# Optimization experiments

Measured on AMD Instinct MI355X. Metric: run time of the kernel, lower is better.

The kernel has to match this reference:

```python
import jax, jax.numpy as jnp
import numpy as np

C, V, T, B = 64, 16000, 64, 8
ALPHA = 1.0  # dt=None -> alpha = 1 (non-trainable buffer)


def setup_inputs() -> dict:
    key = jax.random.key(0)
    k0, k1, k2, k3 = jax.random.split(key, 4)
    tokens = jax.random.randint(k0, (T, B), 0, V)  # time-major [T, B]
    emb_ctx = jax.random.normal(k1, (V, C), dtype=jnp.float32)  # embedding2context
    emb_act = jax.random.normal(k2, (V, C), dtype=jnp.float32)  # embedding2actionable
    bound = 1.0 / np.sqrt(C)
    W_a = jax.random.uniform(k3, (C * V, C), dtype=jnp.float32, minval=-bound, maxval=bound)
    beta_mult = jnp.float32(1.0)
    beta_power = jnp.float32(1.0)
    return {"tokens": tokens, "emb_ctx": emb_ctx, "emb_act": emb_act,
            "W_a": W_a, "beta_mult": beta_mult, "beta_power": beta_power}


def reference(tokens, emb_ctx, emb_act, W_a, beta_mult, beta_power):
    Vv, Cc = emb_ctx.shape
    Tt, Bb = tokens.shape
    # W_a rows are indexed k = v*C + c after .view(-1, V, C)
    W3 = W_a.reshape(Vv, Cc, Cc)  # [V, C, C]

    def step(ctx, tok):
        ce = emb_ctx[tok]  # [B, C] context embedding
        ae = emb_act[tok]  # [B, C] actionable embedding
        ne = jnp.linalg.norm(ce, axis=1, keepdims=True)   # [B, 1]
        nc = jnp.linalg.norm(ctx, axis=1, keepdims=True)  # [B, 1]
        beta = ALPHA * (beta_mult * (ne / (ne + nc))) ** beta_power
        beta = jnp.clip(beta, 0.0, 1.0)
        ctx = (1.0 - beta) * ctx + beta * ce              # norm-gated blend
        # action_map[b,v,c] = sum_d W3[v,c,d] * ctx[b,d]; out[b,v] = sum_c am * ae
        am = jnp.einsum('vcd,bd->bvc', W3, ctx)           # [B, V, C]
        out = jnp.einsum('bvc,bc->bv', am, ae)            # [B, V]
        return ctx, out

    ctx0 = jnp.zeros((Bb, Cc), dtype=emb_ctx.dtype)
    _, outs = jax.lax.scan(step, ctx0, tokens)  # [T, B, V]
    return outs
```

## Files before the change

kernel.cpp:

```cpp
#include <hip/hip_runtime.h>
#include <hip/hip_bf16.h>
#include <stdint.h>

#define T_STEPS 64
#define B_SZ 8
#define C_DIM 64
#define V_SZ 16000
#define K_DIM 4096
#define M_ROWS 512
#define BN 64
#define BK 32
#define NITER (K_DIM / BK)
#define ATILE_BYTES 32768

typedef __bf16 bf16x8 __attribute__((ext_vector_type(8)));
typedef __bf16 bf16x4 __attribute__((ext_vector_type(4)));
typedef float f32x4 __attribute__((ext_vector_type(4)));

__global__ void ctx_kernel(const int* __restrict__ tokens,
                           const float* __restrict__ emb_ctx,
                           const float* __restrict__ beta_mult,
                           const float* __restrict__ beta_power,
                           float* __restrict__ ctx_hist) {
  const int b = blockIdx.x;
  const int d = threadIdx.x;
  const float bm = beta_mult[0];
  const float bp = beta_power[0];
  float ctx = 0.0f;
  for (int t = 0; t < T_STEPS; ++t) {
    const int tok = tokens[t * B_SZ + b];
    const float ce = emb_ctx[tok * C_DIM + d];
    float ne2 = ce * ce;
    float c2 = ctx * ctx;
#pragma unroll
    for (int s = 32; s > 0; s >>= 1) {
      ne2 += __shfl_xor(ne2, s, 64);
      c2 += __shfl_xor(c2, s, 64);
    }
    const float ne = sqrtf(ne2);
    const float nc = sqrtf(c2);
    float beta = powf(bm * (ne / (ne + nc)), bp);
    beta = fminf(fmaxf(beta, 0.0f), 1.0f);
    ctx = (1.0f - beta) * ctx + beta * ce;
    ctx_hist[(t * B_SZ + b) * C_DIM + d] = ctx;
  }
}

__global__ void build_m(const int* __restrict__ tokens,
                        const float* __restrict__ emb_act,
                        const float* __restrict__ ctx_hist,
                        char* __restrict__ Mblk) {
  const int m = blockIdx.x;
  const int tid = threadIdx.x;
  __shared__ float ctxs[C_DIM];
  __shared__ float aes[C_DIM];
  const int t = m >> 3, b = m & 7;
  const int tok = tokens[t * B_SZ + b];
  if (tid < C_DIM) {
    ctxs[tid] = ctx_hist[m * C_DIM + tid];
    aes[tid] = emb_act[tok * C_DIM + tid];
  }
  __syncthreads();
  const int c = tid >> 1;
  const int dh = (tid & 1) * 32;
  const float ae = aes[c];
#pragma unroll
  for (int q = 0; q < 4; ++q) {
    const int k0 = c * C_DIM + dh + q * 8;
    bf16x8 v;
#pragma unroll
    for (int jj = 0; jj < 8; ++jj) v[jj] = (__bf16)(ae * ctxs[dh + q * 8 + jj]);
    *(bf16x8*)(void*)(Mblk + (size_t)(k0 >> 5) * 32768 + ((k0 >> 3) & 3) * 8192 +
                      m * 16) = v;
  }
}

__global__ __launch_bounds__(512, 2)
void gemm_kernel(const char* __restrict__ Ablk, const float* __restrict__ W,
                 float* __restrict__ out) {
  __shared__ char wlds[4][4096];
  const int tid = threadIdx.x;
  const int lane = tid & 63;
  const int w = tid >> 6;
  const int lrow = lane & 15;
  const int g = lane >> 4;
  const int n0 = blockIdx.x * BN;

  int aoff[4];
#pragma unroll
  for (int fm = 0; fm < 4; ++fm)
    aoff[fm] = g * 8192 + (w * 64 + fm * 16 + lrow) * 16;

  const char* const Wc = (const char*)W;
  const size_t wvoff = ((size_t)(n0 + (tid >> 3)) * K_DIM + (tid & 7) * 4) * 4;
  const int wldsoff = ((tid & 7) >> 1) * 1024 + (tid >> 3) * 16 + (tid & 1) * 8;

  f32x4 acc[4][4];
#pragma unroll
  for (int fm = 0; fm < 4; ++fm)
#pragma unroll
    for (int fn = 0; fn < 4; ++fn) acc[fm][fn] = (f32x4){0.f, 0.f, 0.f, 0.f};

  bf16x8 a2[2][4];
  f32x4 wr[4];

  wr[0] = *(const f32x4*)(Wc + wvoff);
  wr[1] = *(const f32x4*)(Wc + wvoff + 128);
#pragma unroll
  for (int fm = 0; fm < 4; ++fm) a2[0][fm] = *(const bf16x8*)(Ablk + aoff[fm]);
  wr[2] = *(const f32x4*)(Wc + wvoff + 256);
  {
    bf16x4 h;
#pragma unroll
    for (int q = 0; q < 4; ++q) h[q] = (__bf16)wr[0][q];
    *(bf16x4*)(wlds[0] + wldsoff) = h;
  }
  asm volatile("s_waitcnt lgkmcnt(0)" ::: "memory");
  __builtin_amdgcn_s_barrier();
  __builtin_amdgcn_sched_barrier(0);

#pragma unroll 1
  for (int bb = 0; bb < NITER / 4; ++bb) {
#pragma unroll
    for (int j = 0; j < 4; ++j) {
      const int kt = bb * 4 + j;
      const int kta = (kt + 1 < NITER) ? kt + 1 : kt;
      const char* ap = Ablk + (size_t)kta * ATILE_BYTES;
#pragma unroll
      for (int fm = 0; fm < 4; ++fm)
        a2[(j + 1) & 1][fm] = *(const bf16x8*)(ap + aoff[fm]);
      const int ktw = (kt + 3 < NITER) ? kt + 3 : NITER - 1;
      wr[(j + 3) & 3] = *(const f32x4*)(Wc + wvoff + (size_t)ktw * 128);
      {
        bf16x4 h;
#pragma unroll
        for (int q = 0; q < 4; ++q) h[q] = (__bf16)wr[(j + 1) & 3][q];
        *(bf16x4*)(wlds[(j + 1) & 3] + wldsoff) = h;
      }
      asm volatile("s_waitcnt lgkmcnt(0)" ::: "memory");
      __builtin_amdgcn_s_barrier();
      __builtin_amdgcn_sched_barrier(0);
#pragma unroll
      for (int fn = 0; fn < 4; ++fn) {
        const bf16x8 bv =
            *(const bf16x8*)(wlds[j & 3] + g * 1024 + (fn * 16 + lrow) * 16);
#pragma unroll
        for (int fm = 0; fm < 4; ++fm)
          acc[fm][fn] = __builtin_amdgcn_mfma_f32_16x16x32_bf16(
              a2[j & 1][fm], bv, acc[fm][fn], 0, 0, 0);
      }
    }
  }

#pragma unroll
  for (int fm = 0; fm < 4; ++fm)
#pragma unroll
    for (int q = 0; q < 4; ++q) {
      const int row = w * 64 + fm * 16 + g * 4 + q;
      float* po = out + (size_t)row * V_SZ + n0 + lrow;
#pragma unroll
      for (int fn = 0; fn < 4; ++fn) po[fn * 16] = acc[fm][fn][q];
    }
}

extern "C" void kernel_launch(void* const* d_in, const int* in_sizes, int n_in,
                              void* d_out, int out_size, void* d_ws, size_t ws_size,
                              hipStream_t stream) {
  const int* tokens = (const int*)d_in[0];
  const float* emb_ctx = (const float*)d_in[1];
  const float* emb_act = (const float*)d_in[2];
  const float* W = (const float*)d_in[3];
  const float* beta_mult = (const float*)d_in[4];
  const float* beta_power = (const float*)d_in[5];
  float* out = (float*)d_out;

  char* Mblk = (char*)d_ws;
  float* ctx_hist = (float*)((char*)d_ws + (size_t)M_ROWS * K_DIM * 2);

  ctx_kernel<<<B_SZ, C_DIM, 0, stream>>>(tokens, emb_ctx, beta_mult, beta_power,
                                         ctx_hist);
  build_m<<<M_ROWS, 128, 0, stream>>>(tokens, emb_act, ctx_hist, Mblk);
  gemm_kernel<<<V_SZ / BN, 512, 0, stream>>>(Mblk, W, out);
}
```

Measured before the change: 175.0 us.

## Stage fp32 W tiles via global_load_lds with swizzle, split M across workgroups

The GEMM now uses 256x128 tiles with the M dimension split across two workgroups and an XCD-aware remapping of block indices. W tiles are copied straight into LDS in fp32 through global_load_lds with an XOR swizzle, and converted to bf16 when read back. The A layout is reorganised into per-half contiguous chunks, and a hand-scheduled 4-slot pipeline uses explicit vmcnt waits and setprio. The goal is to remove register-staged W conversion and LDS writes and to improve overlap of the W stream. The cost is that W is read twice (once per M half), LDS use is larger, and occupancy drops to one block per CU.

After: 208.7 us. 1.19x slower.

```diff
diff --git a/kernel.cpp b/kernel.cpp
--- a/kernel.cpp
+++ b/kernel.cpp
@@ -8,14 +8,21 @@
 #define V_SZ 16000
 #define K_DIM 4096
 #define M_ROWS 512
-#define BN 64
-#define BK 32
-#define NITER (K_DIM / BK)
-#define ATILE_BYTES 32768
+#define BM 256
+#define BN 128
+#define NPH 128
+#define NWG ((M_ROWS / BM) * (V_SZ / BN))
+#define AH_BYTES 16384
+#define WSLOT 16384
 
 typedef __bf16 bf16x8 __attribute__((ext_vector_type(8)));
-typedef __bf16 bf16x4 __attribute__((ext_vector_type(4)));
 typedef float f32x4 __attribute__((ext_vector_type(4)));
+
+__device__ __forceinline__ void gll16(const void* g, void* l) {
+  __builtin_amdgcn_global_load_lds(
+      (const __attribute__((address_space(1))) void*)g,
+      (__attribute__((address_space(3))) void*)l, 16, 0, 0);
+}
 
 __global__ void ctx_kernel(const int* __restrict__ tokens,
                            const float* __restrict__ emb_ctx,
@@ -64,100 +71,144 @@
   const int c = tid >> 1;
   const int dh = (tid & 1) * 32;
   const float ae = aes[c];
+  const size_t base = (size_t)(m >> 8) * 2097152 + (size_t)(m & 255) * 64;
 #pragma unroll
   for (int q = 0; q < 4; ++q) {
     const int k0 = c * C_DIM + dh + q * 8;
     bf16x8 v;
 #pragma unroll
     for (int jj = 0; jj < 8; ++jj) v[jj] = (__bf16)(ae * ctxs[dh + q * 8 + jj]);
-    *(bf16x8*)(void*)(Mblk + (size_t)(k0 >> 5) * 32768 + ((k0 >> 3) & 3) * 8192 +
-                      m * 16) = v;
-  }
-}
-
-__global__ __launch_bounds__(512, 2)
+    *(bf16x8*)(void*)(Mblk + base + (size_t)(k0 >> 5) * AH_BYTES +
+                      (size_t)(k0 & 31) * 2) = v;
+  }
+}
+
+__global__ __launch_bounds__(512, 1)
 void gemm_kernel(const char* __restrict__ Ablk, const float* __restrict__ W,
                  float* __restrict__ out) {
-  __shared__ char wlds[4][4096];
+  __shared__ __align__(16) char wlds[4][WSLOT];
   const int tid = threadIdx.x;
   const int lane = tid & 63;
   const int w = tid >> 6;
+  const int wm = w >> 1, wn = w & 1;
   const int lrow = lane & 15;
   const int g = lane >> 4;
-  const int n0 = blockIdx.x * BN;
-
-  int aoff[4];
+
+  const int orig = blockIdx.x;
+  const int xcd = orig & 7;
+  const int wg = ((xcd < 2) ? xcd * 32 : 64 + (xcd - 2) * 31) + (orig >> 3);
+  const int mi = wg & 1;
+  const int n0 = (wg >> 1) * BN;
+
+  const char* const asb = Ablk + (size_t)mi * 2097152 +
+                          (size_t)(wm * 64 + lrow) * 64 + g * 16;
+  bf16x8 areg[2][4];
+  auto LOAD_A = [&](int s, int h) {
+    const char* ap = asb + (size_t)h * AH_BYTES;
+#pragma unroll
+    for (int fm = 0; fm < 4; ++fm)
+      areg[s][fm] = *(const bf16x8*)(ap + fm * 1024);
+  };
+
+  const char* const Wc = (const char*)W;
+  const int wcol = tid >> 3;
+  const int wkb = ((tid & 7) * 16) ^ ((wcol & 7) << 4);
+  const char* const wsrc0 = Wc + (size_t)(n0 + wcol) * (K_DIM * 4) + wkb;
+  const char* const wsrc1 = wsrc0 + (size_t)64 * (K_DIM * 4);
+  auto STAGE_W = [&](int slot, int h) {
+    gll16(wsrc0 + (size_t)h * 128, &wlds[slot][0] + tid * 16);
+    gll16(wsrc1 + (size_t)h * 128, &wlds[slot][0] + 8192 + tid * 16);
+  };
+
+  f32x4 acc[4][4];
 #pragma unroll
   for (int fm = 0; fm < 4; ++fm)
-    aoff[fm] = g * 8192 + (w * 64 + fm * 16 + lrow) * 16;
-
-  const char* const Wc = (const char*)W;
-  const size_t wvoff = ((size_t)(n0 + (tid >> 3)) * K_DIM + (tid & 7) * 4) * 4;
-  const int wldsoff = ((tid & 7) >> 1) * 1024 + (tid >> 3) * 16 + (tid & 1) * 8;
-
-  f32x4 acc[4][4];
+#pragma unroll
+    for (int fn = 0; fn < 4; ++fn) acc[fm][fn] = (f32x4){0.f, 0.f, 0.f, 0.f};
+
+  const int xo = (lrow & 7) << 4;
+
+  auto COMPUTE = [&](int slot, int s) {
+    const char* Wb = &wlds[slot][0];
+    f32x4 b0[4], b1[4];
+#pragma unroll
+    for (int fn = 0; fn < 4; ++fn) {
+      const char* cb = Wb + (wn * 64 + fn * 16 + lrow) * 128;
+      b0[fn] = *(const f32x4*)(cb + ((g * 32) ^ xo));
+      b1[fn] = *(const f32x4*)(cb + ((g * 32 + 16) ^ xo));
+    }
+    asm volatile("s_waitcnt lgkmcnt(0)" ::: "memory");
+    __builtin_amdgcn_sched_barrier(0);
+    __builtin_amdgcn_s_setprio(1);
+#pragma unroll
+    for (int fn = 0; fn < 4; ++fn) {
+      bf16x8 bv;
+#pragma unroll
+      for (int j = 0; j < 4; ++j) {
+        bv[j] = (__bf16)b0[fn][j];
+        bv[4 + j] = (__bf16)b1[fn][j];
+      }
+#pragma unroll
+      for (int fm = 0; fm < 4; ++fm)
+        acc[fm][fn] = __builtin_amdgcn_mfma_f32_16x16x32_bf16(
+            areg[s][fm], bv, acc[fm][fn], 0, 0, 0);
+    }
+    __builtin_amdgcn_s_setprio(0);
+  };
+
+#define PH_BAR() __builtin_amdgcn_s_barrier()
+
+  LOAD_A(0, 0);
+  STAGE_W(0, 0);
+  STAGE_W(1, 1);
+  STAGE_W(2, 2);
+
+  LOAD_A(1, 1); STAGE_W(3, 3);
+  asm volatile("s_waitcnt vmcnt(10)" ::: "memory");
+  PH_BAR(); COMPUTE(0, 0); PH_BAR();
+  LOAD_A(0, 2); STAGE_W(0, 4);
+  asm volatile("s_waitcnt vmcnt(14)" ::: "memory");
+  PH_BAR(); COMPUTE(1, 1); PH_BAR();
+
+#pragma unroll 1
+  for (int j = 0; j < 30; ++j) {
+    const int pb = 2 + j * 4;
+#pragma unroll
+    for (int u = 0; u < 4; ++u) {
+      const int p = pb + u;
+      LOAD_A((p + 1) & 1, p + 1);
+      STAGE_W((p + 3) & 3, p + 3);
+      asm volatile("s_waitcnt vmcnt(18)" ::: "memory");
+      PH_BAR();
+      COMPUTE(p & 3, p & 1);
+      PH_BAR();
+    }
+  }
+
+  LOAD_A(1, 123); STAGE_W(1, 125);
+  asm volatile("s_waitcnt vmcnt(18)" ::: "memory");
+  PH_BAR(); COMPUTE(2, 0); PH_BAR();
+  LOAD_A(0, 124); STAGE_W(2, 126);
+  asm volatile("s_waitcnt vmcnt(18)" ::: "memory");
+  PH_BAR(); COMPUTE(3, 1); PH_BAR();
+  LOAD_A(1, 125); STAGE_W(3, 127);
+  asm volatile("s_waitcnt vmcnt(18)" ::: "memory");
+  PH_BAR(); COMPUTE(0, 0); PH_BAR();
+  LOAD_A(0, 126);
+  asm volatile("s_waitcnt vmcnt(16)" ::: "memory");
+  PH_BAR(); COMPUTE(1, 1); PH_BAR();
+  LOAD_A(1, 127);
+  asm volatile("s_waitcnt vmcnt(14)" ::: "memory");
+  PH_BAR(); COMPUTE(2, 0); PH_BAR();
+  asm volatile("s_waitcnt vmcnt(8)" ::: "memory");
+  PH_BAR(); COMPUTE(3, 1);
+
 #pragma unroll
   for (int fm = 0; fm < 4; ++fm)
 #pragma unroll
-    for (int fn = 0; fn < 4; ++fn) acc[fm][fn] = (f32x4){0.f, 0.f, 0.f, 0.f};
-
-  bf16x8 a2[2][4];
-  f32x4 wr[4];
-
-  wr[0] = *(const f32x4*)(Wc + wvoff);
-  wr[1] = *(const f32x4*)(Wc + wvoff + 128);
-#pragma unroll
-  for (int fm = 0; fm < 4; ++fm) a2[0][fm] = *(const bf16x8*)(Ablk + aoff[fm]);
-  wr[2] = *(const f32x4*)(Wc + wvoff + 256);
-  {
-    bf16x4 h;
-#pragma unroll
-    for (int q = 0; q < 4; ++q) h[q] = (__bf16)wr[0][q];
-    *(bf16x4*)(wlds[0] + wldsoff) = h;
-  }
-  asm volatile("s_waitcnt lgkmcnt(0)" ::: "memory");
-  __builtin_amdgcn_s_barrier();
-  __builtin_amdgcn_sched_barrier(0);
-
-#pragma unroll 1
-  for (int bb = 0; bb < NITER / 4; ++bb) {
-#pragma unroll
-    for (int j = 0; j < 4; ++j) {
-      const int kt = bb * 4 + j;
-      const int kta = (kt + 1 < NITER) ? kt + 1 : kt;
-      const char* ap = Ablk + (size_t)kta * ATILE_BYTES;
-#pragma unroll
-      for (int fm = 0; fm < 4; ++fm)
-        a2[(j + 1) & 1][fm] = *(const bf16x8*)(ap + aoff[fm]);
-      const int ktw = (kt + 3 < NITER) ? kt + 3 : NITER - 1;
-      wr[(j + 3) & 3] = *(const f32x4*)(Wc + wvoff + (size_t)ktw * 128);
-      {
-        bf16x4 h;
-#pragma unroll
-        for (int q = 0; q < 4; ++q) h[q] = (__bf16)wr[(j + 1) & 3][q];
-        *(bf16x4*)(wlds[(j + 1) & 3] + wldsoff) = h;
-      }
-      asm volatile("s_waitcnt lgkmcnt(0)" ::: "memory");
-      __builtin_amdgcn_s_barrier();
-      __builtin_amdgcn_sched_barrier(0);
-#pragma unroll
-      for (int fn = 0; fn < 4; ++fn) {
-        const bf16x8 bv =
-            *(const bf16x8*)(wlds[j & 3] + g * 1024 + (fn * 16 + lrow) * 16);
-#pragma unroll
-        for (int fm = 0; fm < 4; ++fm)
-          acc[fm][fn] = __builtin_amdgcn_mfma_f32_16x16x32_bf16(
-              a2[j & 1][fm], bv, acc[fm][fn], 0, 0, 0);
-      }
-    }
-  }
-
-#pragma unroll
-  for (int fm = 0; fm < 4; ++fm)
-#pragma unroll
     for (int q = 0; q < 4; ++q) {
-      const int row = w * 64 + fm * 16 + g * 4 + q;
-      float* po = out + (size_t)row * V_SZ + n0 + lrow;
+      const int row = mi * BM + wm * 64 + fm * 16 + g * 4 + q;
+      float* po = out + (size_t)row * V_SZ + n0 + wn * 64 + lrow;
 #pragma unroll
       for (int fn = 0; fn < 4; ++fn) po[fn * 16] = acc[fm][fn][q];
     }
@@ -180,5 +231,5 @@
   ctx_kernel<<<B_SZ, C_DIM, 0, stream>>>(tokens, emb_ctx, beta_mult, beta_power,
                                          ctx_hist);
   build_m<<<M_ROWS, 128, 0, stream>>>(tokens, emb_act, ctx_hist, Mblk);
-  gemm_kernel<<<V_SZ / BN, 512, 0, stream>>>(Mblk, W, out);
-}
+  gemm_kernel<<<NWG, 512, 0, stream>>>(Mblk, W, out);
+}
```
